# Performance work log

Hardware: AMD Instinct MI355X
Metric: run time of the kernel (lower is better)

## Reference

```python
import jax, jax.numpy as jnp
import numpy as np

N, E, H, G, C = 50000, 800000, 512, 64, 2
BERT = 768


def setup_inputs() -> dict:
    key = jax.random.key(0)
    ks = jax.random.split(key, 12)
    sem = jax.random.normal(ks[0], (N, BERT), jnp.float32)
    mask = jax.random.randint(ks[1], (N, 1), 0, 2).astype(jnp.float32)
    x = jnp.concatenate([sem, mask], axis=1)  # [N, 769]
    edge_index = jax.random.randint(ks[2], (2, E), 0, N)
    batch = jnp.sort(jax.random.randint(ks[3], (N,), 0, G))
    s = lambda k, shp, fan: jax.random.normal(k, shp, jnp.float32) / np.float32(np.sqrt(fan))
    return dict(
        x=x, edge_index=edge_index, batch=batch,
        sem_W=s(ks[4], (BERT, H), BERT), sem_b=jnp.zeros((H,), jnp.float32),
        slice_emb=jax.random.normal(ks[5], (2, H), jnp.float32),
        ln_g=jnp.ones((H,), jnp.float32), ln_b=jnp.zeros((H,), jnp.float32),
        conv1_W=s(ks[6], (H, H), H), conv1_b=jnp.zeros((H,), jnp.float32),
        conv2_W=s(ks[7], (H, H), H), conv2_b=jnp.zeros((H,), jnp.float32),
        cls_W1=s(ks[8], (H, H), H), cls_b1=jnp.zeros((H,), jnp.float32),
        cls_W2=s(ks[9], (H, C), H), cls_b2=jnp.zeros((C,), jnp.float32),
    )


def _layer_norm(x, g, b, eps=1e-5):
    m = x.mean(-1, keepdims=True)
    v = x.var(-1, keepdims=True)
    return (x - m) * jax.lax.rsqrt(v + eps) * g + b


def _gcn_conv(h, src, dst, W, b):
    # PyG GCNConv: add self-loops, sym-normalized aggregation of X @ W, plus bias
    hw = h @ W  # [N, H]
    deg = jnp.zeros((N,), hw.dtype).at[dst].add(1.0) + 1.0  # +1 self-loop
    dinv = jax.lax.rsqrt(deg)
    coef = dinv[src] * dinv[dst]  # [E]
    agg = jax.ops.segment_sum(hw[src] * coef[:, None], dst, num_segments=N)
    agg = agg + hw * (dinv * dinv)[:, None]  # self-loop contribution
    return agg + b


def reference(x, edge_index, batch, sem_W, sem_b, slice_emb, ln_g, ln_b,
              conv1_W, conv1_b, conv2_W, conv2_b, cls_W1, cls_b1, cls_W2, cls_b2):
    sem = x[:, :BERT]
    idx = x[:, BERT].astype(jnp.int32)  # binary slice mask
    h = sem @ sem_W + sem_b + slice_emb[idx]
    h = jax.nn.gelu(_layer_norm(h, ln_g, ln_b), approximate=False)
    src, dst = edge_index[0], edge_index[1]
    h = jax.nn.gelu(_gcn_conv(h, src, dst, conv1_W, conv1_b), approximate=False)
    h2 = jax.nn.gelu(_gcn_conv(h, src, dst, conv2_W, conv2_b), approximate=False)
    h = h + h2  # residual (args.residual=True)
    sums = jax.ops.segment_sum(h, batch, num_segments=G)
    cnt = jax.ops.segment_sum(jnp.ones((N,), h.dtype), batch, num_segments=G)
    hg = sums / jnp.maximum(cnt, 1.0)[:, None]  # global mean pool [G, H]
    z = jax.nn.gelu(hg @ cls_W1 + cls_b1, approximate=False)
    return z @ cls_W2 + cls_b2  # [G, C]
```

## Files before the change

### kernel.cpp

```cpp
#include <hip/hip_runtime.h>
#include <hip/hip_bf16.h>

typedef unsigned short u16;
typedef __bf16 bfv8 __attribute__((ext_vector_type(8)));
typedef float f32x4 __attribute__((ext_vector_type(4)));
typedef unsigned int u32x4 __attribute__((ext_vector_type(4)));

#define HH 512
#define BERT_D 768
#define XSTRIDE 769

__device__ __forceinline__ float gelu_f(float x) {
  return 0.5f * x * (1.0f + erff(x * 0.70710678118654752440f));
}
__device__ __forceinline__ float us2f(u16 u) {
  union { unsigned int i; float f; } c; c.i = ((unsigned int)u) << 16; return c.f;
}
__device__ __forceinline__ u16 f2us(float f) {
  union { float f; unsigned int i; } c; c.f = f;
  unsigned int i = c.i;
  i += 0x7FFFu + ((i >> 16) & 1u);
  return (u16)(i >> 16);
}
__device__ __forceinline__ void gl_lds16(const u16* g, u16* l) {
  __builtin_amdgcn_global_load_lds((const __attribute__((address_space(1))) void*)g,
                                   (__attribute__((address_space(3))) void*)l, 16, 0, 0);
}

__global__ void k_idx(const float* __restrict__ x, int* __restrict__ idx, int Nn) {
  int i = blockIdx.x * blockDim.x + threadIdx.x;
  if (i < Nn) idx[i] = (int)x[(size_t)i * XSTRIDE + BERT_D];
}

__global__ void k_transpose_bf16(const float* __restrict__ src, u16* __restrict__ dst,
                                 int K, int Nn) {
  int i = blockIdx.x * blockDim.x + threadIdx.x;
  if (i >= K * Nn) return;
  int k = i / Nn, j = i - k * Nn;
  dst[(size_t)j * K + k] = f2us(src[i]);
}

__global__ void k_deg(const int* __restrict__ dst, int* __restrict__ deg, int E) {
  int e = blockIdx.x * blockDim.x + threadIdx.x;
  if (e < E) atomicAdd(&deg[dst[e]], 1);
}

__launch_bounds__(256)
__global__ void k_part(const int* __restrict__ deg, int* __restrict__ part, int Nn) {
  const int i = blockIdx.x * 256 + threadIdx.x;
  int v = (i < Nn) ? deg[i] : 0;
#pragma unroll
  for (int o = 32; o; o >>= 1) v += __shfl_xor(v, o);
  __shared__ int ws4[4];
  if ((threadIdx.x & 63) == 0) ws4[threadIdx.x >> 6] = v;
  __syncthreads();
  if (threadIdx.x == 0) part[blockIdx.x] = ws4[0] + ws4[1] + ws4[2] + ws4[3];
}

__launch_bounds__(256)
__global__ void k_scan_part(int* __restrict__ part, int* __restrict__ row_ptr,
                            int nb, int Nn) {
  __shared__ int sm[256];
  const int t = threadIdx.x;
  int v = (t < nb) ? part[t] : 0;
  sm[t] = v;
  __syncthreads();
  for (int d = 1; d < 256; d <<= 1) {
    int u = (t >= d) ? sm[t - d] : 0;
    __syncthreads();
    sm[t] += u;
    __syncthreads();
  }
  if (t < nb) part[t] = sm[t] - v;
  if (t == 255) row_ptr[Nn] = sm[255];
}

__launch_bounds__(256)
__global__ void k_scan_write(const int* __restrict__ deg, const int* __restrict__ part,
                             int* __restrict__ row_ptr, int* __restrict__ cursor,
                             float* __restrict__ dinv, int Nn) {
  __shared__ int sm[256];
  const int t = threadIdx.x;
  const int i = blockIdx.x * 256 + t;
  int v = (i < Nn) ? deg[i] : 0;
  sm[t] = v;
  __syncthreads();
  for (int d = 1; d < 256; d <<= 1) {
    int u = (t >= d) ? sm[t - d] : 0;
    __syncthreads();
    sm[t] += u;
    __syncthreads();
  }
  if (i < Nn) {
    int pre = part[blockIdx.x] + sm[t] - v;
    row_ptr[i] = pre;
    cursor[i] = pre;
    dinv[i] = rsqrtf((float)v + 1.0f);
  }
}

__global__ void k_csr(const int* __restrict__ src, const int* __restrict__ dst,
                      int* __restrict__ cursor, int* __restrict__ csr_src, int E) {
  int e = blockIdx.x * blockDim.x + threadIdx.x;
  if (e >= E) return;
  int d = dst[e];
  int pos = atomicAdd(&cursor[d], 1);
  csr_src[pos] = src[e];
}

__launch_bounds__(256, 2)
__global__ void k_gemm1(const float* __restrict__ xf,
                        const u16* __restrict__ B, int ldb,
                        u16* __restrict__ C, int M,
                        const float* __restrict__ bias,
                        const float* __restrict__ emb,
                        const int* __restrict__ idx) {
  __shared__ alignas(16) u16 As[128 * 64];
  __shared__ alignas(16) u16 Bs[256 * 64];
  const int t = threadIdx.x;
  const int l = t & 63;
  const int w = t >> 6;
  const int wro = (w >> 1) * 64;
  const int wco = (w & 1) * 128;
  const int lr = l & 15;
  const int kg = (l >> 4) * 8;
  const int nwg = gridDim.x;
  const int id = blockIdx.x;
  const int q8 = nwg >> 3, r8 = nwg & 7;
  const int xcd = id & 7, rk = id >> 3;
  const int swz = (xcd < r8 ? xcd * (q8 + 1) : r8 * (q8 + 1) + (xcd - r8) * q8) + rk;
  const int brow = (swz >> 1) * 128;
  const int bcol = (swz & 1) * 256;

  const int arr = t >> 4;
  const int ac4 = (t & 15) * 4;

  f32x4 acc[4][8] = {};

  for (int k0 = 0; k0 < BERT_D; k0 += 64) {
#pragma unroll
    for (int i = 0; i < 8; ++i) {
      const int eo = (i * 256 + t) * 8;
      const int r = eo >> 6;
      const int c = eo & 63;
      gl_lds16(B + (size_t)(bcol + r) * ldb + (k0 + c), Bs + eo);
    }
#pragma unroll
    for (int i = 0; i < 8; ++i) {
      const int rr = i * 16 + arr;
      int gr = brow + rr;
      if (gr > M - 1) gr = M - 1;
      const float* xp = xf + (size_t)gr * XSTRIDE + k0 + ac4;
      float f0 = xp[0], f1 = xp[1], f2 = xp[2], f3 = xp[3];
      union { u16 h[4]; unsigned long long q; } pk;
      pk.h[0] = f2us(f0); pk.h[1] = f2us(f1); pk.h[2] = f2us(f2); pk.h[3] = f2us(f3);
      *(unsigned long long*)(As + rr * 64 + ac4) = pk.q;
    }
    __syncthreads();
#pragma unroll
    for (int ks = 0; ks < 2; ++ks) {
      bfv8 af[4], bfr[8];
#pragma unroll
      for (int m = 0; m < 4; ++m)
        af[m] = __builtin_bit_cast(bfv8, *(const uint4*)(As + (wro + m * 16 + lr) * 64 + ks * 32 + kg));
#pragma unroll
      for (int n = 0; n < 8; ++n)
        bfr[n] = __builtin_bit_cast(bfv8, *(const uint4*)(Bs + (wco + n * 16 + lr) * 64 + ks * 32 + kg));
#pragma unroll
      for (int m = 0; m < 4; ++m)
#pragma unroll
        for (int n = 0; n < 8; ++n)
          acc[m][n] = __builtin_amdgcn_mfma_f32_16x16x32_bf16(af[m], bfr[n], acc[m][n], 0, 0, 0);
    }
    __syncthreads();
  }

#pragma unroll
  for (int m = 0; m < 4; ++m) {
#pragma unroll
    for (int r = 0; r < 4; ++r) {
      const int row = brow + wro + m * 16 + (l >> 4) * 4 + r;
      if (row >= M) continue;
#pragma unroll
      for (int n = 0; n < 8; ++n) {
        const int col = bcol + wco + n * 16 + lr;
        float v = acc[m][n][r] + bias[col] + emb[idx[row] * HH + col];
        C[(size_t)row * HH + col] = f2us(v);
      }
    }
  }
}

template <int EPI>
__launch_bounds__(256, 2)
__global__ void k_gemm_bt(const u16* __restrict__ A, int lda,
                          const u16* __restrict__ B, int ldb,
                          u16* __restrict__ C, int M, int Kd,
                          const float* __restrict__ dscale) {
  __shared__ alignas(16) u16 As[128 * 64];
  __shared__ alignas(16) u16 Bs[256 * 64];
  const int t = threadIdx.x;
  const int l = t & 63;
  const int w = t >> 6;
  const int wro = (w >> 1) * 64;
  const int wco = (w & 1) * 128;
  const int lr = l & 15;
  const int kg = (l >> 4) * 8;
  const int nwg = gridDim.x;
  const int id = blockIdx.x;
  const int q8 = nwg >> 3, r8 = nwg & 7;
  const int xcd = id & 7, rk = id >> 3;
  const int swz = (xcd < r8 ? xcd * (q8 + 1) : r8 * (q8 + 1) + (xcd - r8) * q8) + rk;
  const int brow = (swz >> 1) * 128;
  const int bcol = (swz & 1) * 256;

  f32x4 acc[4][8] = {};

  for (int k0 = 0; k0 < Kd; k0 += 64) {
#pragma unroll
    for (int i = 0; i < 4; ++i) {
      const int eo = (i * 256 + t) * 8;
      const int r = eo >> 6;
      const int c = eo & 63;
      int gr = brow + r;
      if (gr > M - 1) gr = M - 1;
      gl_lds16(A + (size_t)gr * lda + (k0 + c), As + eo);
    }
#pragma unroll
    for (int i = 0; i < 8; ++i) {
      const int eo = (i * 256 + t) * 8;
      const int r = eo >> 6;
      const int c = eo & 63;
      gl_lds16(B + (size_t)(bcol + r) * ldb + (k0 + c), Bs + eo);
    }
    __syncthreads();
#pragma unroll
    for (int ks = 0; ks < 2; ++ks) {
      bfv8 af[4], bfr[8];
#pragma unroll
      for (int m = 0; m < 4; ++m)
        af[m] = __builtin_bit_cast(bfv8, *(const uint4*)(As + (wro + m * 16 + lr) * 64 + ks * 32 + kg));
#pragma unroll
      for (int n = 0; n < 8; ++n)
        bfr[n] = __builtin_bit_cast(bfv8, *(const uint4*)(Bs + (wco + n * 16 + lr) * 64 + ks * 32 + kg));
#pragma unroll
      for (int m = 0; m < 4; ++m)
#pragma unroll
        for (int n = 0; n < 8; ++n)
          acc[m][n] = __builtin_amdgcn_mfma_f32_16x16x32_bf16(af[m], bfr[n], acc[m][n], 0, 0, 0);
    }
    __syncthreads();
  }

#pragma unroll
  for (int m = 0; m < 4; ++m) {
#pragma unroll
    for (int r = 0; r < 4; ++r) {
      const int row = brow + wro + m * 16 + (l >> 4) * 4 + r;
      if (row >= M) continue;
      const float sc = (EPI == 2) ? dscale[row] : 1.0f;
#pragma unroll
      for (int n = 0; n < 8; ++n) {
        const int col = bcol + wco + n * 16 + lr;
        float v = acc[m][n][r];
        if (EPI == 2) v *= sc;
        C[(size_t)row * HH + col] = f2us(v);
      }
    }
  }
}

__launch_bounds__(256)
__global__ void k_ln_gelu(const u16* __restrict__ h0, const float* __restrict__ gw,
                          const float* __restrict__ bw, u16* __restrict__ hout, int Nn) {
  const int wid = (int)((blockIdx.x * (long long)blockDim.x + threadIdx.x) >> 6);
  if (wid >= Nn) return;
  const int l = threadIdx.x & 63;
  uint4 q = *(const uint4*)(h0 + (size_t)wid * HH + l * 8);
  const u16* us = (const u16*)&q;
  float f[8]; float s = 0.f, s2 = 0.f;
#pragma unroll
  for (int j = 0; j < 8; ++j) { f[j] = us2f(us[j]); s += f[j]; s2 += f[j] * f[j]; }
#pragma unroll
  for (int o = 32; o; o >>= 1) { s += __shfl_xor(s, o); s2 += __shfl_xor(s2, o); }
  const float mean = s * (1.f / 512.f);
  const float var = s2 * (1.f / 512.f) - mean * mean;
  const float rs = rsqrtf(var + 1e-5f);
  union { u16 ov[8]; uint4 q; } o;
#pragma unroll
  for (int j = 0; j < 8; ++j) {
    int col = l * 8 + j;
    float y = (f[j] - mean) * rs * gw[col] + bw[col];
    o.ov[j] = f2us(gelu_f(y));
  }
  *(uint4*)(hout + (size_t)wid * HH + l * 8) = o.q;
}

__launch_bounds__(256)
__global__ void k_agg(const u16* __restrict__ hwS, const int* __restrict__ row_ptr,
                      const int* __restrict__ csr_src, const float* __restrict__ dinv,
                      const float* __restrict__ bias, u16* __restrict__ hout, int Nn) {
  const int wid = (int)((blockIdx.x * (long long)blockDim.x + threadIdx.x) >> 6);
  if (wid >= Nn) return;
  const int l = threadIdx.x & 63;
  const int cb = l * 8;
  float acc[8] = {0.f, 0.f, 0.f, 0.f, 0.f, 0.f, 0.f, 0.f};
  const int lo = row_ptr[wid], hi = row_ptr[wid + 1];
  const float dv = dinv[wid];
  int e = lo;
  for (; e + 4 <= hi; e += 4) {
    const int u0 = csr_src[e + 0];
    const int u1 = csr_src[e + 1];
    const int u2 = csr_src[e + 2];
    const int u3 = csr_src[e + 3];
    uint4 q0 = *(const uint4*)(hwS + (size_t)u0 * HH + cb);
    uint4 q1 = *(const uint4*)(hwS + (size_t)u1 * HH + cb);
    uint4 q2 = *(const uint4*)(hwS + (size_t)u2 * HH + cb);
    uint4 q3 = *(const uint4*)(hwS + (size_t)u3 * HH + cb);
    const u16* p0 = (const u16*)&q0;
    const u16* p1 = (const u16*)&q1;
    const u16* p2 = (const u16*)&q2;
    const u16* p3 = (const u16*)&q3;
#pragma unroll
    for (int j = 0; j < 8; ++j)
      acc[j] += (us2f(p0[j]) + us2f(p1[j])) + (us2f(p2[j]) + us2f(p3[j]));
  }
  for (; e < hi; ++e) {
    const int u = csr_src[e];
    uint4 q = *(const uint4*)(hwS + (size_t)u * HH + cb);
    const u16* p = (const u16*)&q;
#pragma unroll
    for (int j = 0; j < 8; ++j) acc[j] += us2f(p[j]);
  }
  {
    uint4 q = *(const uint4*)(hwS + (size_t)wid * HH + cb);
    const u16* p = (const u16*)&q;
#pragma unroll
    for (int j = 0; j < 8; ++j) acc[j] += us2f(p[j]);
  }
  union { u16 ov[8]; u32x4 q; } o;
#pragma unroll
  for (int j = 0; j < 8; ++j) {
    float v = acc[j] * dv + bias[cb + j];
    o.ov[j] = f2us(gelu_f(v));
  }
  __builtin_nontemporal_store(o.q, (u32x4*)(hout + (size_t)wid * HH + cb));
}

#define POOL_RS 16
__launch_bounds__(256)
__global__ void k_pool2(const u16* __restrict__ h1, const u16* __restrict__ h2,
                        const int* __restrict__ batch, float* __restrict__ hg, int Nn) {
  const int g = blockIdx.x;
  const int chunk = blockIdx.y;
  const int t = threadIdx.x;
  const int w = t >> 6;
  const int l = t & 63;
  const int cb = l * 8;
  int lo, hi;
  { int a = 0, b = Nn; while (a < b) { int m = (a + b) >> 1; if (batch[m] < g) a = m + 1; else b = m; } lo = a; }
  { int a = 0, b = Nn; while (a < b) { int m = (a + b) >> 1; if (batch[m] < g + 1) a = m + 1; else b = m; } hi = a; }
  const int len = hi - lo;
  const int per = (len + POOL_RS - 1) / POOL_RS;
  const int rlo = lo + chunk * per;
  const int rhi = min(rlo + per, hi);
  float acc[8] = {};
  for (int r = rlo + w; r < rhi; r += 4) {
    u32x4 a = __builtin_nontemporal_load((const u32x4*)(h1 + (size_t)r * HH + cb));
    u32x4 b = __builtin_nontemporal_load((const u32x4*)(h2 + (size_t)r * HH + cb));
    const u16* ua = (const u16*)&a;
    const u16* ub = (const u16*)&b;
#pragma unroll
    for (int j = 0; j < 8; ++j) acc[j] += us2f(ua[j]) + us2f(ub[j]);
  }
  __shared__ float red[4][HH];
#pragma unroll
  for (int j = 0; j < 8; ++j) red[w][cb + j] = acc[j];
  __syncthreads();
  if (w == 0) {
#pragma unroll
    for (int j = 0; j < 8; ++j) {
      const int col = cb + j;
      float s = red[0][col] + red[1][col] + red[2][col] + red[3][col];
      if (s != 0.f) atomicAdd(&hg[(size_t)g * HH + col], s);
    }
  }
}

__launch_bounds__(256)
__global__ void k_cls(const float* __restrict__ hg, const int* __restrict__ batch,
                      const float* __restrict__ W1, const float* __restrict__ b1,
                      const float* __restrict__ W2, const float* __restrict__ b2,
                      float* __restrict__ out, int Nn) {
  const int g = blockIdx.x;
  const int t = threadIdx.x;
  __shared__ float hl[512];
  __shared__ float zl[512];
  __shared__ float pr[512];
  int lo, hi;
  { int a = 0, b = Nn; while (a < b) { int m = (a + b) >> 1; if (batch[m] < g) a = m + 1; else b = m; } lo = a; }
  { int a = 0, b = Nn; while (a < b) { int m = (a + b) >> 1; if (batch[m] < g + 1) a = m + 1; else b = m; } hi = a; }
  const float inv = 1.0f / fmaxf((float)(hi - lo), 1.0f);
  hl[t] = hg[(size_t)g * HH + t] * inv;
  hl[t + 256] = hg[(size_t)g * HH + t + 256] * inv;
  __syncthreads();
#pragma unroll
  for (int jj = 0; jj < 2; ++jj) {
    const int j = t + jj * 256;
    float a = b1[j];
    for (int k = 0; k < 512; ++k) a += hl[k] * W1[k * HH + j];
    zl[j] = gelu_f(a);
  }
  __syncthreads();
  float p0 = 0.f, p1 = 0.f;
  for (int k = t; k < 512; k += 256) { p0 += zl[k] * W2[k * 2]; p1 += zl[k] * W2[k * 2 + 1]; }
  pr[t] = p0; pr[t + 256] = p1;
  __syncthreads();
  for (int s2 = 128; s2; s2 >>= 1) {
    if (t < s2) { pr[t] += pr[t + s2]; pr[t + 256] += pr[t + 256 + s2]; }
    __syncthreads();
  }
  if (t == 0) { out[g * 2] = pr[0] + b2[0]; out[g * 2 + 1] = pr[256] + b2[1]; }
}

extern "C" void kernel_launch(void* const* d_in, const int* in_sizes, int n_in,
                              void* d_out, int out_size, void* d_ws, size_t ws_size,
                              hipStream_t stream) {
  const float* x        = (const float*)d_in[0];
  const int*   eidx     = (const int*)d_in[1];
  const int*   batch    = (const int*)d_in[2];
  const float* sem_W    = (const float*)d_in[3];
  const float* sem_b    = (const float*)d_in[4];
  const float* sl_emb   = (const float*)d_in[5];
  const float* ln_g     = (const float*)d_in[6];
  const float* ln_b     = (const float*)d_in[7];
  const float* W1       = (const float*)d_in[8];
  const float* b1       = (const float*)d_in[9];
  const float* W2       = (const float*)d_in[10];
  const float* b2       = (const float*)d_in[11];
  const float* cW1      = (const float*)d_in[12];
  const float* cb1      = (const float*)d_in[13];
  const float* cW2      = (const float*)d_in[14];
  const float* cb2      = (const float*)d_in[15];
  const int N_ = in_sizes[2];
  const int E_ = in_sizes[1] / 2;
  const int G_ = out_size / 2;
  const int* src = eidx;
  const int* dst = eidx + E_;

  char* ws = (char*)d_ws;
  size_t off = 0;
  auto alloc = [&](size_t bytes) -> void* {
    void* p = (void*)(ws + off);
    off += (bytes + 255) & ~(size_t)255;
    return p;
  };
  u16* h1 = (u16*)alloc((size_t)N_ * HH * sizeof(u16));
  u16* h0 = (u16*)alloc((size_t)N_ * HH * sizeof(u16));
  u16* hw = h0;
  u16* h = (u16*)alloc((size_t)N_ * HH * sizeof(u16));
  u16* h2 = h;
  u16* semW_T = (u16*)alloc((size_t)HH * BERT_D * sizeof(u16));
  u16* W1T    = (u16*)alloc((size_t)HH * HH * sizeof(u16));
  u16* W2T    = (u16*)alloc((size_t)HH * HH * sizeof(u16));
  int* idx     = (int*)alloc((size_t)N_ * 4);
  int* deg     = (int*)alloc((size_t)N_ * 4);
  float* dinv  = (float*)alloc((size_t)N_ * 4);
  int* row_ptr = (int*)alloc((size_t)(N_ + 1) * 4);
  int* cursor  = (int*)alloc((size_t)N_ * 4);
  int* csr_src = (int*)alloc((size_t)E_ * 4);
  int* part    = (int*)alloc(1024);
  float* hg    = (float*)alloc((size_t)G_ * HH * 4);

  hipMemsetAsync(deg, 0, (size_t)N_ * 4, stream);
  hipMemsetAsync(hg, 0, (size_t)G_ * HH * 4, stream);

  k_idx<<<(N_ + 255) / 256, 256, 0, stream>>>(x, idx, N_);
  k_transpose_bf16<<<(BERT_D * HH + 255) / 256, 256, 0, stream>>>(sem_W, semW_T, BERT_D, HH);
  k_transpose_bf16<<<(HH * HH + 255) / 256, 256, 0, stream>>>(W1, W1T, HH, HH);
  k_transpose_bf16<<<(HH * HH + 255) / 256, 256, 0, stream>>>(W2, W2T, HH, HH);

  const int nb = (N_ + 255) / 256;
  k_deg<<<(E_ + 255) / 256, 256, 0, stream>>>(dst, deg, E_);
  k_part<<<nb, 256, 0, stream>>>(deg, part, N_);
  k_scan_part<<<1, 256, 0, stream>>>(part, row_ptr, nb, N_);
  k_scan_write<<<nb, 256, 0, stream>>>(deg, part, row_ptr, cursor, dinv, N_);
  k_csr<<<(E_ + 255) / 256, 256, 0, stream>>>(src, dst, cursor, csr_src, E_);

  const int Mtiles = (N_ + 127) / 128;
  const int wave_blocks = (N_ + 3) / 4;
  const int gemm_grid = Mtiles * 2;

  k_gemm1<<<gemm_grid, 256, 0, stream>>>(
      x, semW_T, BERT_D, h0, N_, sem_b, sl_emb, idx);
  k_ln_gelu<<<wave_blocks, 256, 0, stream>>>(h0, ln_g, ln_b, h, N_);
  k_gemm_bt<2><<<gemm_grid, 256, 0, stream>>>(
      h, HH, W1T, HH, hw, N_, HH, dinv);
  k_agg<<<wave_blocks, 256, 0, stream>>>(hw, row_ptr, csr_src, dinv, b1, h1, N_);
  k_gemm_bt<2><<<gemm_grid, 256, 0, stream>>>(
      h1, HH, W2T, HH, hw, N_, HH, dinv);
  k_agg<<<wave_blocks, 256, 0, stream>>>(hw, row_ptr, csr_src, dinv, b2, h2, N_);
  k_pool2<<<dim3(G_, POOL_RS), 256, 0, stream>>>(h1, h2, batch, hg, N_);
  k_cls<<<G_, 256, 0, stream>>>(hg, batch, cW1, cb1, cW2, cb2, (float*)d_out, N_);
}
```

Measured before the change: 725.3 us.

## Halve GEMM K-tile, XOR-swizzle LDS layout, and raise occupancy target

Both MFMA GEMM kernels now stage 32-wide K slices instead of 64, halving shared memory per block. The LDS layout uses an XOR swizzle of the 16-byte chunk index by row, applied consistently on the global-to-LDS write and on the fragment read, to cut bank conflicts on the fragment loads. Launch bounds rise from 2 to 4 blocks per CU to allow more overlap between memory and math. The catch is twice as many barriers per K step and a tighter register budget against 128 accumulator floats per thread, which could cause spills.

```diff
diff --git a/kernel.cpp b/kernel.cpp
--- a/kernel.cpp
+++ b/kernel.cpp
@@ -108,22 +108,24 @@
   csr_src[pos] = src[e];
 }
 
-__launch_bounds__(256, 2)
+
+__launch_bounds__(256, 4)
 __global__ void k_gemm1(const float* __restrict__ xf,
                         const u16* __restrict__ B, int ldb,
                         u16* __restrict__ C, int M,
                         const float* __restrict__ bias,
                         const float* __restrict__ emb,
                         const int* __restrict__ idx) {
-  __shared__ alignas(16) u16 As[128 * 64];
-  __shared__ alignas(16) u16 Bs[256 * 64];
+  __shared__ alignas(16) u16 As[128 * 32];
+  __shared__ alignas(16) u16 Bs[256 * 32];
   const int t = threadIdx.x;
   const int l = t & 63;
   const int w = t >> 6;
   const int wro = (w >> 1) * 64;
   const int wco = (w & 1) * 128;
   const int lr = l & 15;
-  const int kg = (l >> 4) * 8;
+  const int kq = l >> 4;
+  const int rsw = (lr >> 1) & 3;
   const int nwg = gridDim.x;
   const int id = blockIdx.x;
   const int q8 = nwg >> 3, r8 = nwg & 7;
@@ -132,40 +134,37 @@
   const int brow = (swz >> 1) * 128;
   const int bcol = (swz & 1) * 256;
 
-  const int arr = t >> 4;
-  const int ac4 = (t & 15) * 4;
+  const int ssw8 = (((t & 3) ^ ((t >> 3) & 3)) * 8);
+  const int str = t >> 2;
 
   f32x4 acc[4][8] = {};
 
-  for (int k0 = 0; k0 < BERT_D; k0 += 64) {
-#pragma unroll
-    for (int i = 0; i < 8; ++i) {
-      const int eo = (i * 256 + t) * 8;
-      const int r = eo >> 6;
-      const int c = eo & 63;
-      gl_lds16(B + (size_t)(bcol + r) * ldb + (k0 + c), Bs + eo);
-    }
-#pragma unroll
-    for (int i = 0; i < 8; ++i) {
-      const int rr = i * 16 + arr;
-      int gr = brow + rr;
-      if (gr > M - 1) gr = M - 1;
-      const float* xp = xf + (size_t)gr * XSTRIDE + k0 + ac4;
-      float f0 = xp[0], f1 = xp[1], f2 = xp[2], f3 = xp[3];
-      union { u16 h[4]; unsigned long long q; } pk;
-      pk.h[0] = f2us(f0); pk.h[1] = f2us(f1); pk.h[2] = f2us(f2); pk.h[3] = f2us(f3);
-      *(unsigned long long*)(As + rr * 64 + ac4) = pk.q;
-    }
-    __syncthreads();
-#pragma unroll
-    for (int ks = 0; ks < 2; ++ks) {
+  for (int k0 = 0; k0 < BERT_D; k0 += 32) {
+#pragma unroll
+    for (int i = 0; i < 4; ++i) {
+      const int r = i * 64 + str;
+      gl_lds16(B + (size_t)(bcol + r) * ldb + (k0 + ssw8), Bs + (i * 256 + t) * 8);
+    }
+#pragma unroll
+    for (int i = 0; i < 2; ++i) {
+      const int rr = i * 64 + str;
+      int gr = brow + rr; if (gr > M - 1) gr = M - 1;
+      const float* xp = xf + (size_t)gr * XSTRIDE + k0 + ssw8;
+      union { u16 h[8]; uint4 q; } pk;
+#pragma unroll
+      for (int e = 0; e < 8; ++e) pk.h[e] = f2us(xp[e]);
+      *(uint4*)(As + (i * 256 + t) * 8) = pk.q;
+    }
+    __syncthreads();
+    {
+      const int rg = (kq ^ rsw) * 8;
       bfv8 af[4], bfr[8];
 #pragma unroll
       for (int m = 0; m < 4; ++m)
-        af[m] = __builtin_bit_cast(bfv8, *(const uint4*)(As + (wro + m * 16 + lr) * 64 + ks * 32 + kg));
+        af[m] = __builtin_bit_cast(bfv8, *(const uint4*)(As + (wro + m * 16 + lr) * 32 + rg));
 #pragma unroll
       for (int n = 0; n < 8; ++n)
-        bfr[n] = __builtin_bit_cast(bfv8, *(const uint4*)(Bs + (wco + n * 16 + lr) * 64 + ks * 32 + kg));
+        bfr[n] = __builtin_bit_cast(bfv8, *(const uint4*)(Bs + (wco + n * 16 + lr) * 32 + rg));
 #pragma unroll
       for (int m = 0; m < 4; ++m)
 #pragma unroll
@@ -192,20 +191,21 @@
 }
 
 template <int EPI>
-__launch_bounds__(256, 2)
+__launch_bounds__(256, 4)
 __global__ void k_gemm_bt(const u16* __restrict__ A, int lda,
                           const u16* __restrict__ B, int ldb,
                           u16* __restrict__ C, int M, int Kd,
                           const float* __restrict__ dscale) {
-  __shared__ alignas(16) u16 As[128 * 64];
-  __shared__ alignas(16) u16 Bs[256 * 64];
+  __shared__ alignas(16) u16 As[128 * 32];
+  __shared__ alignas(16) u16 Bs[256 * 32];
   const int t = threadIdx.x;
   const int l = t & 63;
   const int w = t >> 6;
   const int wro = (w >> 1) * 64;
   const int wco = (w & 1) * 128;
   const int lr = l & 15;
-  const int kg = (l >> 4) * 8;
+  const int kq = l >> 4;
+  const int rsw = (lr >> 1) & 3;
   const int nwg = gridDim.x;
   const int id = blockIdx.x;
   const int q8 = nwg >> 3, r8 = nwg & 7;
@@ -214,35 +214,33 @@
   const int brow = (swz >> 1) * 128;
   const int bcol = (swz & 1) * 256;
 
+  const int ssw8 = (((t & 3) ^ ((t >> 3) & 3)) * 8);
+  const int str = t >> 2;
+
   f32x4 acc[4][8] = {};
 
-  for (int k0 = 0; k0 < Kd; k0 += 64) {
+  for (int k0 = 0; k0 < Kd; k0 += 32) {
+#pragma unroll
+    for (int i = 0; i < 2; ++i) {
+      const int r = i * 64 + str;
+      int gr = brow + r; if (gr > M - 1) gr = M - 1;
+      gl_lds16(A + (size_t)gr * lda + (k0 + ssw8), As + (i * 256 + t) * 8);
+    }
 #pragma unroll
     for (int i = 0; i < 4; ++i) {
-      const int eo = (i * 256 + t) * 8;
-      const int r = eo >> 6;
-      const int c = eo & 63;
-      int gr = brow + r;
-      if (gr > M - 1) gr = M - 1;
-      gl_lds16(A + (size_t)gr * lda + (k0 + c), As + eo);
-    }
-#pragma unroll
-    for (int i = 0; i < 8; ++i) {
-      const int eo = (i * 256 + t) * 8;
-      const int r = eo >> 6;
-      const int c = eo & 63;
-      gl_lds16(B + (size_t)(bcol + r) * ldb + (k0 + c), Bs + eo);
-    }
-    __syncthreads();
-#pragma unroll
-    for (int ks = 0; ks < 2; ++ks) {
+      const int r = i * 64 + str;
+      gl_lds16(B + (size_t)(bcol + r) * ldb + (k0 + ssw8), Bs + (i * 256 + t) * 8);
+    }
+    __syncthreads();
+    {
+      const int rg = (kq ^ rsw) * 8;
       bfv8 af[4], bfr[8];
 #pragma unroll
       for (int m = 0; m < 4; ++m)
-        af[m] = __builtin_bit_cast(bfv8, *(const uint4*)(As + (wro + m * 16 + lr) * 64 + ks * 32 + kg));
+        af[m] = __builtin_bit_cast(bfv8, *(const uint4*)(As + (wro + m * 16 + lr) * 32 + rg));
 #pragma unroll
       for (int n = 0; n < 8; ++n)
-        bfr[n] = __builtin_bit_cast(bfv8, *(const uint4*)(Bs + (wco + n * 16 + lr) * 64 + ks * 32 + kg));
+        bfr[n] = __builtin_bit_cast(bfv8, *(const uint4*)(Bs + (wco + n * 16 + lr) * 32 + rg));
 #pragma unroll
       for (int m = 0; m < 4; ++m)
 #pragma unroll
```

After: 1.822 ms. 151% more time.
